# Optimization experiments

Hardware: AMD Instinct MI355X
Metric: run time of the kernel (lower is better)

Reference implementation:

```python
import jax, jax.numpy as jnp
import numpy as np

B, N, E, H, ET = 1, 50000, 600000, 128, 8
EPS = 1e-5


def setup_inputs() -> dict:
    key = jax.random.key(0)
    ks = jax.random.split(key, 20)
    s = 1.0 / np.sqrt(H)
    s2 = 1.0 / np.sqrt(2 * H)
    u = lambda k, shape, b: jax.random.uniform(k, shape, jnp.float32, -b, b)
    return {
        "hidden": jax.random.normal(ks[0], (B, N, H), jnp.float32),
        "edge_index": jax.random.randint(ks[1], (2, E), 0, N),
        "edge_type": jax.random.randint(ks[2], (E,), 0, ET),
        "edge_emb": jax.random.normal(ks[3], (ET, H), jnp.float32),
        "Wq": u(ks[4], (H, H), s), "bq": u(ks[5], (H,), s),
        "Wk": u(ks[6], (H, H), s), "bk": u(ks[7], (H,), s),
        "Wv": u(ks[8], (H, H), s), "bv": u(ks[9], (H,), s),
        "Web": u(ks[10], (H, 1), s), "beb": u(ks[11], (1,), s),
        "W1": u(ks[12], (2 * H, H), s2), "b1": u(ks[13], (H,), s2),
        "W2": u(ks[14], (H, H), s), "b2": u(ks[15], (H,), s),
        "gamma": jnp.ones((H,), jnp.float32),
        "beta": jnp.zeros((H,), jnp.float32),
    }


def reference(hidden, edge_index, edge_type, edge_emb, Wq, bq, Wk, bk, Wv, bv,
              Web, beb, W1, b1, W2, b2, gamma, beta):
    source, target = edge_index[0], edge_index[1]
    src_h = hidden[:, source]                      # [B,E,H] gather
    tgt_h = hidden[:, target]                      # [B,E,H] gather
    eh = edge_emb[edge_type]                       # [E,H]

    q = tgt_h @ Wq + bq                            # [B,E,H]
    sk = src_h + eh[None]                          # [B,E,H]
    k = sk @ Wk + bk
    v = sk @ Wv + bv

    logits = (q * k).sum(-1) / np.sqrt(H)          # [B,E]
    logits = logits + (eh @ Web + beb)[:, 0][None] # edge bias, same across batch

    # segment softmax over incoming edges per target node
    lt = logits.T                                  # [E,B]
    mx = jax.ops.segment_max(lt, target, num_segments=N)   # [N,B]
    ex = jnp.exp(lt - mx[target])
    sm = jax.ops.segment_sum(ex, target, num_segments=N)   # [N,B]
    w = (ex / sm[target]).T                        # [B,E]

    messages = v * w[..., None]                    # [B,E,H]
    agg = jax.ops.segment_sum(jnp.moveaxis(messages, 1, 0), target,
                              num_segments=N)      # [N,B,H]
    agg = jnp.moveaxis(agg, 0, 1)                  # [B,N,H]

    h = jnp.concatenate([hidden, agg], axis=-1)    # [B,N,2H]
    upd = jax.nn.silu(h @ W1 + b1) @ W2 + b2

    x = hidden + upd
    mu = x.mean(-1, keepdims=True)
    var = ((x - mu) ** 2).mean(-1, keepdims=True)
    return (x - mu) / jnp.sqrt(var + EPS) * gamma + beta
```

## Files before the change

kernel.cpp:

```cpp
#include <hip/hip_runtime.h>
#include <math.h>

#define NN 50000
#define NPAD 50048
#define NE 600000
#define H 128
#define ET 8
#define EPS 1e-5f
#define INVSQ 0.08838834764831845f

typedef __attribute__((ext_vector_type(8))) short bf16x8;
typedef __attribute__((ext_vector_type(8))) unsigned short u16x8;
typedef __attribute__((ext_vector_type(4))) float f32x4;

static __device__ inline float bf_lo(unsigned int w) { return __uint_as_float(w << 16); }
static __device__ inline float bf_hi(unsigned int w) { return __uint_as_float(w & 0xFFFF0000u); }
static __device__ inline unsigned short f2bf(float f) {
  unsigned int u = __float_as_uint(f);
  return (unsigned short)((u + 0x7FFFu + ((u >> 16) & 1u)) >> 16);
}

#define PH_B 3125
#define PW_B 384
#define ET_B 8
#define HIST_B 2344

__global__ __launch_bounds__(256) void prep_all_kernel(
    const float* __restrict__ hidden, const float* __restrict__ edge_emb,
    const float* __restrict__ Wq, const float* __restrict__ Wk, const float* __restrict__ Wv,
    const float* __restrict__ W1, const float* __restrict__ W2,
    const float* __restrict__ Web, const float* __restrict__ beb,
    const int* __restrict__ tgt,
    unsigned short* __restrict__ hcat, unsigned short* __restrict__ WqkvT,
    unsigned short* __restrict__ W1T, unsigned short* __restrict__ W2T,
    uint2* __restrict__ KVe, float* __restrict__ ebuf, int* __restrict__ deg) {
  __shared__ float lbuf[256];
  const int blk = blockIdx.x;
  const int t = threadIdx.x;
  if (blk < PH_B) {
    int g = blk * 256 + t;
    int row = g >> 4, seg = g & 15;
    const float4* src = (const float4*)(hidden + (size_t)row * 128 + seg * 8);
    float4 x0 = src[0], x1 = src[1];
    u16x8 o;
    o[0] = f2bf(x0.x); o[1] = f2bf(x0.y); o[2] = f2bf(x0.z); o[3] = f2bf(x0.w);
    o[4] = f2bf(x1.x); o[5] = f2bf(x1.y); o[6] = f2bf(x1.z); o[7] = f2bf(x1.w);
    *(u16x8*)(hcat + (size_t)row * 256 + seg * 8) = o;
  } else if (blk < PH_B + PW_B) {
    int idx = (blk - PH_B) * 256 + t;
    if (idx < 49152) {
      int r = idx >> 7, k = idx & 127;
      const float* W = (r < 128) ? Wq : (r < 256) ? Wk : Wv;
      WqkvT[idx] = f2bf(W[k * 128 + (r & 127)]);
    } else if (idx < 81920) {
      int j = idx - 49152;
      int r = j >> 8, k = j & 255;
      W1T[j] = f2bf(W1[k * 128 + r]);
    } else if (idx < 98304) {
      int j = idx - 81920;
      int r = j >> 7, k = j & 127;
      W2T[j] = f2bf(W2[k * 128 + r]);
    }
  } else if (blk < PH_B + PW_B + ET_B) {
    int e = blk - (PH_B + PW_B);
    if (t < 128) {
      float sk = 0.f, sv = 0.f;
      for (int i = 0; i < 128; ++i) {
        float ev = edge_emb[e * 128 + i];
        sk = fmaf(ev, Wk[i * 128 + t], sk);
        sv = fmaf(ev, Wv[i * 128 + t], sv);
      }
      lbuf[t] = sk;
      lbuf[128 + t] = sv;
    } else if (t == 192) {
      float s2 = beb[0];
      for (int i = 0; i < 128; ++i) s2 = fmaf(edge_emb[e * 128 + i], Web[i], s2);
      ebuf[e] = s2;
    }
    __syncthreads();
    if (t >= 128 && t < 192) {
      int l = t - 128;
      unsigned int kp = (unsigned int)f2bf(lbuf[2 * l]) | ((unsigned int)f2bf(lbuf[2 * l + 1]) << 16);
      unsigned int vp = (unsigned int)f2bf(lbuf[128 + 2 * l]) | ((unsigned int)f2bf(lbuf[128 + 2 * l + 1]) << 16);
      uint2 p; p.x = kp; p.y = vp;
      KVe[e * 64 + l] = p;
    }
  } else {
    int e = (blk - (PH_B + PW_B + ET_B)) * 256 + t;
    if (e < NE) atomicAdd(&deg[tgt[e]], 1);
  }
}

__global__ __launch_bounds__(256) void qkv_mfma_kernel(
    const unsigned short* __restrict__ hcat, const unsigned short* __restrict__ WqkvT,
    const float* __restrict__ bq, const float* __restrict__ bk, const float* __restrict__ bv,
    unsigned short* __restrict__ Qb, unsigned short* __restrict__ KV_u16) {
  __shared__ unsigned short stage[64][392];
  const int tid = threadIdx.x;
  const int w = tid >> 6, l = tid & 63;
  const int lr = l & 15, lg = l >> 4;
  const int blk = blockIdx.x;

  f32x4 acc[4][6] = {};
  const unsigned short* Ab = hcat + (size_t)(blk * 64 + lr) * 256 + lg * 8;
  const unsigned short* Bb = WqkvT + (size_t)(w * 96 + lr) * 128 + lg * 8;
#pragma unroll
  for (int ks = 0; ks < 4; ++ks) {
    bf16x8 a[4];
#pragma unroll
    for (int mt = 0; mt < 4; ++mt) a[mt] = *(const bf16x8*)(Ab + mt * 16 * 256 + ks * 32);
#pragma unroll
    for (int ct = 0; ct < 6; ++ct) {
      bf16x8 b = *(const bf16x8*)(Bb + ct * 16 * 128 + ks * 32);
#pragma unroll
      for (int mt = 0; mt < 4; ++mt)
        acc[mt][ct] = __builtin_amdgcn_mfma_f32_16x16x32_bf16(a[mt], b, acc[mt][ct], 0, 0, 0);
    }
  }
#pragma unroll
  for (int ct = 0; ct < 6; ++ct) {
    int c = w * 96 + ct * 16 + lr;
    float bias = (c < 128) ? bq[c] : (c < 256) ? bk[c - 128] : bv[c - 256];
    float sc = (c < 128) ? INVSQ : 1.f;
    int off;
    if (c < 128) off = c;
    else if (c < 256) { int j = c - 128; off = 128 + ((j >> 1) << 2) + (j & 1); }
    else { int j = c - 256; off = 128 + ((j >> 1) << 2) + 2 + (j & 1); }
#pragma unroll
    for (int mt = 0; mt < 4; ++mt)
#pragma unroll
      for (int j = 0; j < 4; ++j)
        stage[mt * 16 + lg * 4 + j][off] = f2bf((acc[mt][ct][j] + bias) * sc);
  }
  __syncthreads();
  for (int idx = tid; idx < 64 * 48; idx += 256) {
    int r = idx / 48, g = idx % 48;
    int row = blk * 64 + r;
    if (row >= NN) continue;
    u16x8 v = *(const u16x8*)(&stage[r][g * 8]);
    if (g < 16) *(u16x8*)(Qb + (size_t)row * 128 + g * 8) = v;
    else *(u16x8*)(KV_u16 + (size_t)row * 256 + (g - 16) * 8) = v;
  }
}

__global__ __launch_bounds__(256) void scan1_kernel(const int* __restrict__ deg,
                                                    int* __restrict__ excl,
                                                    int* __restrict__ sums) {
  __shared__ int buf[256];
  int idx = blockIdx.x * 256 + threadIdx.x;
  int v = (idx < NN) ? deg[idx] : 0;
  buf[threadIdx.x] = v;
  __syncthreads();
  for (int o = 1; o < 256; o <<= 1) {
    int tv = (threadIdx.x >= o) ? buf[threadIdx.x - o] : 0;
    __syncthreads();
    buf[threadIdx.x] += tv;
    __syncthreads();
  }
  if (idx < NN) excl[idx] = buf[threadIdx.x] - v;
  if (threadIdx.x == 255) sums[blockIdx.x] = buf[255];
}

__global__ __launch_bounds__(256) void scan2_kernel(int* __restrict__ sums, int nb) {
  __shared__ int buf[256];
  int v = (threadIdx.x < nb) ? sums[threadIdx.x] : 0;
  buf[threadIdx.x] = v;
  __syncthreads();
  for (int o = 1; o < 256; o <<= 1) {
    int tv = (threadIdx.x >= o) ? buf[threadIdx.x - o] : 0;
    __syncthreads();
    buf[threadIdx.x] += tv;
    __syncthreads();
  }
  if (threadIdx.x < nb) sums[threadIdx.x] = buf[threadIdx.x] - v;
}

__global__ __launch_bounds__(256) void scan3_kernel(const int* __restrict__ excl,
                                                    const int* __restrict__ sums,
                                                    int* __restrict__ row_off,
                                                    int* __restrict__ cursor) {
  int idx = blockIdx.x * 256 + threadIdx.x;
  if (idx < NN) {
    int r = excl[idx] + sums[blockIdx.x];
    row_off[idx] = r;
    cursor[idx] = r;
  }
  if (idx == 0) row_off[NN] = NE;
}

__global__ void scatter_kernel(const int* __restrict__ src, const int* __restrict__ tgt,
                               const int* __restrict__ et, int* __restrict__ cursor,
                               int* __restrict__ packed) {
  int e = blockIdx.x * blockDim.x + threadIdx.x;
  if (e < NE) {
    int pos = atomicAdd(&cursor[tgt[e]], 1);
    packed[pos] = src[e] | (et[e] << 16);
  }
}

__global__ __launch_bounds__(256) void attn_kernel(
    const unsigned int* __restrict__ Qb, const uint2* __restrict__ KV,
    const uint2* __restrict__ KVe, const float* __restrict__ eb,
    const int* __restrict__ row_off, const int* __restrict__ packed,
    unsigned int* __restrict__ hcat_u32) {
  const int wid = (blockIdx.x * blockDim.x + threadIdx.x) >> 6;
  const int lane = threadIdx.x & 63;
  if (wid >= NN) return;
  const int beg = row_off[wid], end = row_off[wid + 1];
  unsigned int qw = Qb[(size_t)wid * 64 + lane];
  const float q0 = bf_lo(qw), q1 = bf_hi(qw);
  float sA = 0.f, a0A = 0.f, a1A = 0.f;
  float sB = 0.f, a0B = 0.f, a1B = 0.f;
  for (int i = beg; i < end; i += 2) {
    int p0 = packed[i];
    bool has1 = (i + 1) < end;
    int p1 = packed[has1 ? i + 1 : i];
    int s0 = p0 & 0xFFFF, t0 = p0 >> 16;
    int s1 = p1 & 0xFFFF, t1 = p1 >> 16;
    uint2 kv0 = KV[(size_t)s0 * 64 + lane];
    uint2 kv1 = KV[(size_t)s1 * 64 + lane];
    uint2 ke0 = KVe[t0 * 64 + lane];
    uint2 ke1 = KVe[t1 * 64 + lane];
    float eb0 = eb[t0], eb1 = eb[t1];
    float part0 = (bf_lo(kv0.x) + bf_lo(ke0.x)) * q0 + (bf_hi(kv0.x) + bf_hi(ke0.x)) * q1;
    float part1 = (bf_lo(kv1.x) + bf_lo(ke1.x)) * q0 + (bf_hi(kv1.x) + bf_hi(ke1.x)) * q1;
#pragma unroll
    for (int o = 32; o >= 1; o >>= 1) {
      part0 += __shfl_xor(part0, o);
      part1 += __shfl_xor(part1, o);
    }
    float pe0 = __expf(part0 + eb0);
    float pe1 = has1 ? __expf(part1 + eb1) : 0.f;
    sA += pe0;
    sB += pe1;
    a0A = fmaf(pe0, bf_lo(kv0.y) + bf_lo(ke0.y), a0A);
    a1A = fmaf(pe0, bf_hi(kv0.y) + bf_hi(ke0.y), a1A);
    a0B = fmaf(pe1, bf_lo(kv1.y) + bf_lo(ke1.y), a0B);
    a1B = fmaf(pe1, bf_hi(kv1.y) + bf_hi(ke1.y), a1B);
  }
  float s = sA + sB;
  float inv = (s > 0.f) ? 1.f / s : 0.f;
  unsigned int lo = f2bf((a0A + a0B) * inv);
  unsigned int hi = f2bf((a1A + a1B) * inv);
  hcat_u32[(size_t)wid * 128 + 64 + lane] = lo | (hi << 16);
}

__global__ __launch_bounds__(256) void ffn_mfma_kernel(
    const unsigned short* __restrict__ hcat, const float* __restrict__ hidden,
    const unsigned short* __restrict__ W1T, const unsigned short* __restrict__ W2T,
    const float* __restrict__ b1, const float* __restrict__ b2,
    const float* __restrict__ gamma, const float* __restrict__ beta,
    float* __restrict__ out) {
  __shared__ unsigned short mid[64][136];
  const int tid = threadIdx.x;
  const int w = tid >> 6, l = tid & 63;
  const int lr = l & 15, lg = l >> 4;
  const int m0 = blockIdx.x * 64 + w * 16;

  f32x4 acc[8] = {};
  const unsigned short* Ab = hcat + (size_t)(m0 + lr) * 256 + lg * 8;
  const unsigned short* Bb = W1T + (size_t)lr * 256 + lg * 8;
#pragma unroll
  for (int ks = 0; ks < 8; ++ks) {
    bf16x8 a = *(const bf16x8*)(Ab + ks * 32);
#pragma unroll
    for (int ct = 0; ct < 8; ++ct) {
      bf16x8 b = *(const bf16x8*)(Bb + ct * 16 * 256 + ks * 32);
      acc[ct] = __builtin_amdgcn_mfma_f32_16x16x32_bf16(a, b, acc[ct], 0, 0, 0);
    }
  }
#pragma unroll
  for (int ct = 0; ct < 8; ++ct) {
    int c = ct * 16 + lr;
    float bb = b1[c];
#pragma unroll
    for (int j = 0; j < 4; ++j) {
      float x = acc[ct][j] + bb;
      float sl = x / (1.f + __expf(-x));
      mid[w * 16 + lg * 4 + j][c] = f2bf(sl);
    }
  }
  __syncthreads();

  f32x4 acc2[8] = {};
  const unsigned short* A2 = &mid[w * 16 + lr][0] + lg * 8;
  const unsigned short* B2 = W2T + (size_t)lr * 128 + lg * 8;
#pragma unroll
  for (int ks = 0; ks < 4; ++ks) {
    bf16x8 a = *(const bf16x8*)(A2 + ks * 32);
#pragma unroll
    for (int ct = 0; ct < 8; ++ct) {
      bf16x8 b = *(const bf16x8*)(B2 + ct * 16 * 128 + ks * 32);
      acc2[ct] = __builtin_amdgcn_mfma_f32_16x16x32_bf16(a, b, acc2[ct], 0, 0, 0);
    }
  }

  float ga[8], be[8], x[8][4];
#pragma unroll
  for (int ct = 0; ct < 8; ++ct) {
    int c = ct * 16 + lr;
    ga[ct] = gamma[c];
    be[ct] = beta[c];
    float bb = b2[c];
#pragma unroll
    for (int j = 0; j < 4; ++j) {
      int r = m0 + lg * 4 + j;
      float h = (r < NN) ? hidden[(size_t)r * 128 + c] : 0.f;
      x[ct][j] = acc2[ct][j] + bb + h;
    }
  }
#pragma unroll
  for (int j = 0; j < 4; ++j) {
    float s = 0.f, ss = 0.f;
#pragma unroll
    for (int ct = 0; ct < 8; ++ct) {
      s += x[ct][j];
      ss += x[ct][j] * x[ct][j];
    }
#pragma unroll
    for (int o = 8; o >= 1; o >>= 1) {
      s += __shfl_xor(s, o);
      ss += __shfl_xor(ss, o);
    }
    float mu = s * (1.f / 128.f);
    float inv = rsqrtf(ss * (1.f / 128.f) - mu * mu + EPS);
    int r = m0 + lg * 4 + j;
    if (r < NN) {
#pragma unroll
      for (int ct = 0; ct < 8; ++ct) {
        int c = ct * 16 + lr;
        out[(size_t)r * 128 + c] = (x[ct][j] - mu) * inv * ga[ct] + be[ct];
      }
    }
  }
}

extern "C" void kernel_launch(void* const* d_in, const int* in_sizes, int n_in,
                              void* d_out, int out_size, void* d_ws, size_t ws_size,
                              hipStream_t stream) {
  const float* hidden = (const float*)d_in[0];
  const int* edge_index = (const int*)d_in[1];
  const int* edge_type = (const int*)d_in[2];
  const float* edge_emb = (const float*)d_in[3];
  const float* Wq = (const float*)d_in[4];
  const float* bq = (const float*)d_in[5];
  const float* Wk = (const float*)d_in[6];
  const float* bk = (const float*)d_in[7];
  const float* Wv = (const float*)d_in[8];
  const float* bv = (const float*)d_in[9];
  const float* Web = (const float*)d_in[10];
  const float* beb = (const float*)d_in[11];
  const float* W1 = (const float*)d_in[12];
  const float* b1 = (const float*)d_in[13];
  const float* W2 = (const float*)d_in[14];
  const float* b2 = (const float*)d_in[15];
  const float* gamma = (const float*)d_in[16];
  const float* beta = (const float*)d_in[17];
  float* out = (float*)d_out;

  const int* srcp = edge_index;
  const int* tgtp = edge_index + NE;

  size_t off = 0;
  auto alloc = [&](size_t bytes) {
    void* p = (char*)d_ws + off;
    off += (bytes + 255) & ~(size_t)255;
    return p;
  };
  unsigned short* hcat = (unsigned short*)alloc((size_t)NPAD * 256 * 2);
  unsigned short* Qb = (unsigned short*)alloc((size_t)NPAD * 128 * 2);
  unsigned short* KV = (unsigned short*)alloc((size_t)NPAD * 256 * 2);
  unsigned short* WqkvT = (unsigned short*)alloc(384 * 128 * 2);
  unsigned short* W1T = (unsigned short*)alloc(128 * 256 * 2);
  unsigned short* W2T = (unsigned short*)alloc(128 * 128 * 2);
  uint2* KVe = (uint2*)alloc(ET * 64 * 8);
  float* eb = (float*)alloc(ET * 4);
  int* deg = (int*)alloc((size_t)NN * 4);
  int* excl = (int*)alloc((size_t)NN * 4);
  int* sums = (int*)alloc(256 * 4);
  int* row_off = (int*)alloc((size_t)(NN + 1) * 4);
  int* cursor = (int*)alloc((size_t)NN * 4);
  int* packed = (int*)alloc((size_t)NE * 4);

  hipMemsetAsync(deg, 0, (size_t)NN * 4, stream);

  const int scan_blocks = (NN + 255) / 256;

  prep_all_kernel<<<PH_B + PW_B + ET_B + HIST_B, 256, 0, stream>>>(
      hidden, edge_emb, Wq, Wk, Wv, W1, W2, Web, beb, tgtp, hcat, WqkvT, W1T, W2T, KVe, eb, deg);
  scan1_kernel<<<scan_blocks, 256, 0, stream>>>(deg, excl, sums);
  scan2_kernel<<<1, 256, 0, stream>>>(sums, scan_blocks);
  scan3_kernel<<<scan_blocks, 256, 0, stream>>>(excl, sums, row_off, cursor);
  scatter_kernel<<<(NE + 255) / 256, 256, 0, stream>>>(srcp, tgtp, edge_type, cursor, packed);
  qkv_mfma_kernel<<<NPAD / 64, 256, 0, stream>>>(hcat, WqkvT, bq, bk, bv, Qb, KV);
  attn_kernel<<<(NN * 64 + 255) / 256, 256, 0, stream>>>(
      (const unsigned int*)Qb, (const uint2*)KV, KVe, eb, row_off, packed,
      (unsigned int*)hcat);
  ffn_mfma_kernel<<<NPAD / 64, 256, 0, stream>>>(hcat, hidden, W1T, W2T, b1, b2, gamma, beta,
                                                 out);
}
```

Baseline: 327.2 us.

## Precompute per-node edge-type key terms and process four edges per wave in attention

Uses the identity q·(k_src + k_et) = q·k_src + q·k_et: a new kernel precomputes q·Ke[et] + edge bias for each node and each of the 8 edge types, so the attention loop no longer adds the edge-type key per edge. The attention kernel now splits the wave into four 16-lane groups, each handling one edge with 8 features per lane and uint4 loads, and uses 4-step shuffles instead of 6. The groups' partial sums are combined at the end. Edge-type K/V embeddings are kept in fp32, which costs one extra kernel launch and a per-node qke buffer in exchange for less per-edge work and better memory-level parallelism.

```diff
diff --git a/kernel.cpp b/kernel.cpp
--- a/kernel.cpp
+++ b/kernel.cpp
@@ -15,6 +15,9 @@
 
 static __device__ inline float bf_lo(unsigned int w) { return __uint_as_float(w << 16); }
 static __device__ inline float bf_hi(unsigned int w) { return __uint_as_float(w & 0xFFFF0000u); }
+static __device__ inline float bfu(unsigned short v) {
+  return __uint_as_float((unsigned int)v << 16);
+}
 static __device__ inline unsigned short f2bf(float f) {
   unsigned int u = __float_as_uint(f);
   return (unsigned short)((u + 0x7FFFu + ((u >> 16) & 1u)) >> 16);
@@ -33,8 +36,8 @@
     const int* __restrict__ tgt,
     unsigned short* __restrict__ hcat, unsigned short* __restrict__ WqkvT,
     unsigned short* __restrict__ W1T, unsigned short* __restrict__ W2T,
-    uint2* __restrict__ KVe, float* __restrict__ ebuf, int* __restrict__ deg) {
-  __shared__ float lbuf[256];
+    float* __restrict__ Kef, float* __restrict__ Vef, float* __restrict__ ebuf,
+    int* __restrict__ deg) {
   const int blk = blockIdx.x;
   const int t = threadIdx.x;
   if (blk < PH_B) {
@@ -70,20 +73,12 @@
         sk = fmaf(ev, Wk[i * 128 + t], sk);
         sv = fmaf(ev, Wv[i * 128 + t], sv);
       }
-      lbuf[t] = sk;
-      lbuf[128 + t] = sv;
-    } else if (t == 192) {
+      Kef[e * 128 + t] = sk;
+      Vef[e * 128 + t] = sv;
+    } else if (t == 128) {
       float s2 = beb[0];
       for (int i = 0; i < 128; ++i) s2 = fmaf(edge_emb[e * 128 + i], Web[i], s2);
       ebuf[e] = s2;
-    }
-    __syncthreads();
-    if (t >= 128 && t < 192) {
-      int l = t - 128;
-      unsigned int kp = (unsigned int)f2bf(lbuf[2 * l]) | ((unsigned int)f2bf(lbuf[2 * l + 1]) << 16);
-      unsigned int vp = (unsigned int)f2bf(lbuf[128 + 2 * l]) | ((unsigned int)f2bf(lbuf[128 + 2 * l + 1]) << 16);
-      uint2 p; p.x = kp; p.y = vp;
-      KVe[e * 64 + l] = p;
     }
   } else {
     int e = (blk - (PH_B + PW_B + ET_B)) * 256 + t;
@@ -141,6 +136,32 @@
     if (g < 16) *(u16x8*)(Qb + (size_t)row * 128 + g * 8) = v;
     else *(u16x8*)(KV_u16 + (size_t)row * 256 + (g - 16) * 8) = v;
   }
+}
+
+__global__ __launch_bounds__(256) void qke_kernel(const unsigned short* __restrict__ Qb,
+                                                  const float* __restrict__ Kef,
+                                                  const float* __restrict__ ebuf,
+                                                  float* __restrict__ qke) {
+  const int wid = (blockIdx.x * 256 + threadIdx.x) >> 6;
+  const int lane = threadIdx.x & 63;
+  const int et = lane >> 3, part = lane & 7;
+  const unsigned short* q = Qb + (size_t)wid * 128 + part * 16;
+  u16x8 q0 = *(const u16x8*)q;
+  u16x8 q1 = *(const u16x8*)(q + 8);
+  const float4* kf = (const float4*)(Kef + et * 128 + part * 16);
+  float4 k0 = kf[0], k1 = kf[1], k2 = kf[2], k3 = kf[3];
+  float d = 0.f;
+  d = fmaf(bfu(q0[0]), k0.x, d); d = fmaf(bfu(q0[1]), k0.y, d);
+  d = fmaf(bfu(q0[2]), k0.z, d); d = fmaf(bfu(q0[3]), k0.w, d);
+  d = fmaf(bfu(q0[4]), k1.x, d); d = fmaf(bfu(q0[5]), k1.y, d);
+  d = fmaf(bfu(q0[6]), k1.z, d); d = fmaf(bfu(q0[7]), k1.w, d);
+  d = fmaf(bfu(q1[0]), k2.x, d); d = fmaf(bfu(q1[1]), k2.y, d);
+  d = fmaf(bfu(q1[2]), k2.z, d); d = fmaf(bfu(q1[3]), k2.w, d);
+  d = fmaf(bfu(q1[4]), k3.x, d); d = fmaf(bfu(q1[5]), k3.y, d);
+  d = fmaf(bfu(q1[6]), k3.z, d); d = fmaf(bfu(q1[7]), k3.w, d);
+#pragma unroll
+  for (int o = 4; o >= 1; o >>= 1) d += __shfl_xor(d, o);
+  if (part == 0) qke[(size_t)wid * 8 + et] = d + ebuf[et];
 }
 
 __global__ __launch_bounds__(256) void scan1_kernel(const int* __restrict__ deg,
@@ -199,50 +220,66 @@
 }
 
 __global__ __launch_bounds__(256) void attn_kernel(
-    const unsigned int* __restrict__ Qb, const uint2* __restrict__ KV,
-    const uint2* __restrict__ KVe, const float* __restrict__ eb,
+    const unsigned short* __restrict__ Qb, const uint4* __restrict__ KV4,
+    const float* __restrict__ qke, const float* __restrict__ Vef,
     const int* __restrict__ row_off, const int* __restrict__ packed,
-    unsigned int* __restrict__ hcat_u32) {
+    unsigned short* __restrict__ hcat_u16) {
   const int wid = (blockIdx.x * blockDim.x + threadIdx.x) >> 6;
   const int lane = threadIdx.x & 63;
-  if (wid >= NN) return;
+  const int g = lane >> 4, m = lane & 15;
   const int beg = row_off[wid], end = row_off[wid + 1];
-  unsigned int qw = Qb[(size_t)wid * 64 + lane];
-  const float q0 = bf_lo(qw), q1 = bf_hi(qw);
-  float sA = 0.f, a0A = 0.f, a1A = 0.f;
-  float sB = 0.f, a0B = 0.f, a1B = 0.f;
-  for (int i = beg; i < end; i += 2) {
-    int p0 = packed[i];
-    bool has1 = (i + 1) < end;
-    int p1 = packed[has1 ? i + 1 : i];
-    int s0 = p0 & 0xFFFF, t0 = p0 >> 16;
-    int s1 = p1 & 0xFFFF, t1 = p1 >> 16;
-    uint2 kv0 = KV[(size_t)s0 * 64 + lane];
-    uint2 kv1 = KV[(size_t)s1 * 64 + lane];
-    uint2 ke0 = KVe[t0 * 64 + lane];
-    uint2 ke1 = KVe[t1 * 64 + lane];
-    float eb0 = eb[t0], eb1 = eb[t1];
-    float part0 = (bf_lo(kv0.x) + bf_lo(ke0.x)) * q0 + (bf_hi(kv0.x) + bf_hi(ke0.x)) * q1;
-    float part1 = (bf_lo(kv1.x) + bf_lo(ke1.x)) * q0 + (bf_hi(kv1.x) + bf_hi(ke1.x)) * q1;
-#pragma unroll
-    for (int o = 32; o >= 1; o >>= 1) {
-      part0 += __shfl_xor(part0, o);
-      part1 += __shfl_xor(part1, o);
-    }
-    float pe0 = __expf(part0 + eb0);
-    float pe1 = has1 ? __expf(part1 + eb1) : 0.f;
-    sA += pe0;
-    sB += pe1;
-    a0A = fmaf(pe0, bf_lo(kv0.y) + bf_lo(ke0.y), a0A);
-    a1A = fmaf(pe0, bf_hi(kv0.y) + bf_hi(ke0.y), a1A);
-    a0B = fmaf(pe1, bf_lo(kv1.y) + bf_lo(ke1.y), a0B);
-    a1B = fmaf(pe1, bf_hi(kv1.y) + bf_hi(ke1.y), a1B);
-  }
-  float s = sA + sB;
-  float inv = (s > 0.f) ? 1.f / s : 0.f;
-  unsigned int lo = f2bf((a0A + a0B) * inv);
-  unsigned int hi = f2bf((a1A + a1B) * inv);
-  hcat_u32[(size_t)wid * 128 + 64 + lane] = lo | (hi << 16);
+  u16x8 qv = *(const u16x8*)(Qb + (size_t)wid * 128 + m * 8);
+  float q[8];
+#pragma unroll
+  for (int j = 0; j < 8; ++j) q[j] = bfu(qv[j]);
+  const float* qkb = qke + (size_t)wid * 8;
+  float a[8] = {0.f, 0.f, 0.f, 0.f, 0.f, 0.f, 0.f, 0.f};
+  float s = 0.f;
+  for (int i = beg; i < end; i += 4) {
+    int ii = i + g;
+    bool valid = ii < end;
+    int p = packed[valid ? ii : beg];
+    int src = p & 0xFFFF, et = p >> 16;
+    const uint4* row = KV4 + (size_t)src * 32 + m * 2;
+    uint4 x0 = row[0], x1 = row[1];
+    float d;
+    d = bf_lo(x0.x) * q[0];
+    d = fmaf(bf_hi(x0.x), q[1], d);
+    d = fmaf(bf_lo(x0.z), q[2], d);
+    d = fmaf(bf_hi(x0.z), q[3], d);
+    d = fmaf(bf_lo(x1.x), q[4], d);
+    d = fmaf(bf_hi(x1.x), q[5], d);
+    d = fmaf(bf_lo(x1.z), q[6], d);
+    d = fmaf(bf_hi(x1.z), q[7], d);
+#pragma unroll
+    for (int o = 8; o >= 1; o >>= 1) d += __shfl_xor(d, o);
+    float pe = __expf(d + qkb[et]);
+    pe = valid ? pe : 0.f;
+    s += pe;
+    const float4* vef = (const float4*)(Vef + et * 128 + m * 8);
+    float4 v0 = vef[0], v1 = vef[1];
+    a[0] = fmaf(pe, bf_lo(x0.y) + v0.x, a[0]);
+    a[1] = fmaf(pe, bf_hi(x0.y) + v0.y, a[1]);
+    a[2] = fmaf(pe, bf_lo(x0.w) + v0.z, a[2]);
+    a[3] = fmaf(pe, bf_hi(x0.w) + v0.w, a[3]);
+    a[4] = fmaf(pe, bf_lo(x1.y) + v1.x, a[4]);
+    a[5] = fmaf(pe, bf_hi(x1.y) + v1.y, a[5]);
+    a[6] = fmaf(pe, bf_lo(x1.w) + v1.z, a[6]);
+    a[7] = fmaf(pe, bf_hi(x1.w) + v1.w, a[7]);
+  }
+#pragma unroll
+  for (int o = 16; o <= 32; o <<= 1) {
+    s += __shfl_xor(s, o);
+#pragma unroll
+    for (int j = 0; j < 8; ++j) a[j] += __shfl_xor(a[j], o);
+  }
+  if (g == 0) {
+    float inv = (s > 0.f) ? 1.f / s : 0.f;
+    u16x8 o;
+#pragma unroll
+    for (int j = 0; j < 8; ++j) o[j] = f2bf(a[j] * inv);
+    *(u16x8*)(hcat_u16 + (size_t)wid * 256 + 128 + m * 8) = o;
+  }
 }
 
 __global__ __launch_bounds__(256) void ffn_mfma_kernel(
@@ -373,8 +410,10 @@
   unsigned short* WqkvT = (unsigned short*)alloc(384 * 128 * 2);
   unsigned short* W1T = (unsigned short*)alloc(128 * 256 * 2);
   unsigned short* W2T = (unsigned short*)alloc(128 * 128 * 2);
-  uint2* KVe = (uint2*)alloc(ET * 64 * 8);
-  float* eb = (float*)alloc(ET * 4);
+  float* Kef = (float*)alloc(ET * H * 4);
+  float* Vef = (float*)alloc(ET * H * 4);
+  float* ebuf = (float*)alloc(ET * 4);
+  float* qke = (float*)alloc((size_t)NN * 8 * 4);
   int* deg = (int*)alloc((size_t)NN * 4);
   int* excl = (int*)alloc((size_t)NN * 4);
   int* sums = (int*)alloc(256 * 4);
@@ -387,15 +426,16 @@
   const int scan_blocks = (NN + 255) / 256;
 
   prep_all_kernel<<<PH_B + PW_B + ET_B + HIST_B, 256, 0, stream>>>(
-      hidden, edge_emb, Wq, Wk, Wv, W1, W2, Web, beb, tgtp, hcat, WqkvT, W1T, W2T, KVe, eb, deg);
+      hidden, edge_emb, Wq, Wk, Wv, W1, W2, Web, beb, tgtp, hcat, WqkvT, W1T, W2T, Kef, Vef,
+      ebuf, deg);
   scan1_kernel<<<scan_blocks, 256, 0, stream>>>(deg, excl, sums);
   scan2_kernel<<<1, 256, 0, stream>>>(sums, scan_blocks);
   scan3_kernel<<<scan_blocks, 256, 0, stream>>>(excl, sums, row_off, cursor);
   scatter_kernel<<<(NE + 255) / 256, 256, 0, stream>>>(srcp, tgtp, edge_type, cursor, packed);
   qkv_mfma_kernel<<<NPAD / 64, 256, 0, stream>>>(hcat, WqkvT, bq, bk, bv, Qb, KV);
-  attn_kernel<<<(NN * 64 + 255) / 256, 256, 0, stream>>>(
-      (const unsigned int*)Qb, (const uint2*)KV, KVe, eb, row_off, packed,
-      (unsigned int*)hcat);
+  qke_kernel<<<NN / 4, 256, 0, stream>>>(Qb, Kef, ebuf, qke);
+  attn_kernel<<<(NN * 64) / 256, 256, 0, stream>>>(Qb, (const uint4*)KV, qke, Vef, row_off,
+                                                   packed, hcat);
   ffn_mfma_kernel<<<NPAD / 64, 256, 0, stream>>>(hcat, hidden, W1T, W2T, b1, b2, gamma, beta,
                                                  out);
 }
```

Measured after the change: 333.3 us. About the same (+1.8%).
